# Kernel optimization log

Measured on AMD Instinct MI355X. Metric: run time of the kernel, lower is better.

The kernel has to match this reference:

```python
import jax, jax.numpy as jnp
import numpy as np

DIM = 768
HEADS = 12
HEAD_DIM = DIM // HEADS
HIDDEN = int(DIM * 4.0)
EPS = 1e-5


def _layernorm(x, g, b):
    mu = jnp.mean(x, axis=-1, keepdims=True)
    var = jnp.mean(jnp.square(x - mu), axis=-1, keepdims=True)
    return (x - mu) * jax.lax.rsqrt(var + EPS) * g + b


def setup_inputs() -> dict:
    key = jax.random.key(0)
    ks = jax.random.split(key, 8)
    s_in = 1.0 / np.sqrt(DIM)
    s_hid = 1.0 / np.sqrt(HIDDEN)
    return {
        "x": jax.random.normal(ks[0], (2, 2048, DIM), dtype=jnp.float32),
        "ln1_g": jnp.ones((DIM,), jnp.float32),
        "ln1_b": jnp.zeros((DIM,), jnp.float32),
        "w_qkv": jax.random.normal(ks[1], (DIM, 3 * DIM), jnp.float32) * s_in,
        "w_proj": jax.random.normal(ks[2], (DIM, DIM), jnp.float32) * s_in,
        "b_proj": jnp.zeros((DIM,), jnp.float32),
        "ln2_g": jnp.ones((DIM,), jnp.float32),
        "ln2_b": jnp.zeros((DIM,), jnp.float32),
        "w_fc1": jax.random.normal(ks[3], (DIM, HIDDEN), jnp.float32) * s_in,
        "b_fc1": jnp.zeros((HIDDEN,), jnp.float32),
        "w_fc2": jax.random.normal(ks[4], (HIDDEN, DIM), jnp.float32) * s_hid,
        "b_fc2": jnp.zeros((DIM,), jnp.float32),
    }


def reference(x, ln1_g, ln1_b, w_qkv, w_proj, b_proj, ln2_g, ln2_b, w_fc1, b_fc1, w_fc2, b_fc2):
    b, n, c = x.shape
    scale = HEAD_DIM ** -0.5

    # --- attention branch ---
    h = _layernorm(x, ln1_g, ln1_b)
    qkv = (h @ w_qkv).reshape(b, n, 3, HEADS, HEAD_DIM)
    q, k, v = jnp.moveaxis(qkv, 2, 0)          # each [b, n, H, hd]
    attn = jnp.einsum("bqhd,bkhd->bhqk", q, k) * scale
    attn = jax.nn.softmax(attn, axis=-1)       # [b, H, n, n] (naive, materialized)
    o = jnp.einsum("bhqk,bkhd->bqhd", attn, v).reshape(b, n, c)
    x = x + o @ w_proj + b_proj

    # --- MLP branch ---
    h2 = _layernorm(x, ln2_g, ln2_b)
    m = jax.nn.gelu(h2 @ w_fc1 + b_fc1, approximate=False)
    x = x + m @ w_fc2 + b_fc2
    return x
```

## Files before the change

kernel.cpp:

```cpp
#include <hip/hip_runtime.h>
#include <math.h>


typedef unsigned short u16;
typedef __attribute__((ext_vector_type(8))) short short8;
typedef __attribute__((ext_vector_type(4))) float f32x4;

#define TOKENS 4096
#define DIM    768
#define QKV_N  2304
#define HID    3072
#define NSEQ   2048
#define NHEAD  12
#define HDIM   64

__device__ __forceinline__ float bf2f(u16 u) {
  union { unsigned i; float f; } v; v.i = ((unsigned)u) << 16; return v.f;
}
__device__ __forceinline__ u16 f2bf(float f) {
  union { float f; unsigned i; } v; v.f = f;
  unsigned r = v.i + 0x7fffu + ((v.i >> 16) & 1u);
  return (u16)(r >> 16);
}
__device__ __forceinline__ u16 f2bf_trunc(float f) {
  union { float f; unsigned i; } v; v.f = f;
  return (u16)(v.i >> 16);
}

__device__ __forceinline__ void async_copy16(const u16* g, u16* l) {
  __builtin_amdgcn_global_load_lds(
      (const __attribute__((address_space(1))) unsigned int*)(unsigned long long)g,
      (__attribute__((address_space(3))) unsigned int*)(unsigned int)(unsigned long long)l,
      16, 0, 0);
}

__global__ __launch_bounds__(256) void transpose_all(
    const float* __restrict__ in0, u16* __restrict__ out0,
    const float* __restrict__ in1, u16* __restrict__ out1,
    const float* __restrict__ in2, u16* __restrict__ out2,
    const float* __restrict__ in3, u16* __restrict__ out3) {
  __shared__ u16 t[32][33];
  int bid = blockIdx.x, rem;
  const float* in; u16* out; int R, C;
  if (bid < 1728)      { in = in0; out = out0; R = 768;  C = 2304; rem = bid; }
  else if (bid < 2304) { in = in1; out = out1; R = 768;  C = 768;  rem = bid - 1728; }
  else if (bid < 4608) { in = in2; out = out2; R = 768;  C = 3072; rem = bid - 2304; }
  else                 { in = in3; out = out3; R = 3072; C = 768;  rem = bid - 4608; }
  int c0 = (rem % (C / 32)) * 32, r0 = (rem / (C / 32)) * 32;
  int tx = threadIdx.x, ty = threadIdx.y;
#pragma unroll
  for (int i = 0; i < 4; i++)
    t[ty + i * 8][tx] = f2bf(in[(size_t)(r0 + ty + i * 8) * C + c0 + tx]);
  __syncthreads();
#pragma unroll
  for (int i = 0; i < 4; i++)
    out[(size_t)(c0 + ty + i * 8) * R + r0 + tx] = t[tx][ty + i * 8];
}

__global__ __launch_bounds__(256) void transpose_v(const u16* __restrict__ qkv,
                                                   u16* __restrict__ vt) {
  __shared__ u16 t[32][33];
  int c0 = blockIdx.x * 32;
  int r0 = blockIdx.y * 32;
  int tx = threadIdx.x, ty = threadIdx.y;
#pragma unroll
  for (int i = 0; i < 4; i++)
    t[ty + i * 8][tx] = qkv[(size_t)(r0 + ty + i * 8) * QKV_N + 2 * DIM + c0 + tx];
  __syncthreads();
  int b = r0 >> 11, tok = (r0 & 2047) + tx;
#pragma unroll
  for (int i = 0; i < 4; i++)
    vt[((size_t)b * DIM + c0 + ty + i * 8) * NSEQ + tok] = t[tx][ty + i * 8];
}

template <bool INF32>
__global__ __launch_bounds__(256) void ln_kernel(const void* __restrict__ xin,
                                                 const float* __restrict__ g,
                                                 const float* __restrict__ b,
                                                 u16* __restrict__ out) {
  int wave = threadIdx.x >> 6, lane = threadIdx.x & 63;
  int token = blockIdx.x * 4 + wave;
  float v[12];
  if (INF32) {
    const float4* xr = (const float4*)((const float*)xin + (size_t)token * DIM);
#pragma unroll
    for (int w = 0; w < 3; w++) {
      float4 q = xr[lane + w * 64];
      v[w * 4 + 0] = q.x; v[w * 4 + 1] = q.y; v[w * 4 + 2] = q.z; v[w * 4 + 3] = q.w;
    }
  } else {
    const ushort4* xr = (const ushort4*)((const u16*)xin + (size_t)token * DIM);
#pragma unroll
    for (int w = 0; w < 3; w++) {
      ushort4 q = xr[lane + w * 64];
      v[w * 4 + 0] = bf2f(q.x); v[w * 4 + 1] = bf2f(q.y);
      v[w * 4 + 2] = bf2f(q.z); v[w * 4 + 3] = bf2f(q.w);
    }
  }
  float s = 0.f;
#pragma unroll
  for (int i = 0; i < 12; i++) s += v[i];
#pragma unroll
  for (int off = 32; off > 0; off >>= 1) s += __shfl_xor(s, off);
  float mu = s * (1.0f / DIM);
  float ss = 0.f;
#pragma unroll
  for (int i = 0; i < 12; i++) { float d = v[i] - mu; ss += d * d; }
#pragma unroll
  for (int off = 32; off > 0; off >>= 1) ss += __shfl_xor(ss, off);
  float rs = rsqrtf(ss * (1.0f / DIM) + 1e-5f);

  ushort4* orow = (ushort4*)(out + (size_t)token * DIM);
  const float4* g4 = (const float4*)g;
  const float4* b4 = (const float4*)b;
#pragma unroll
  for (int w = 0; w < 3; w++) {
    float4 gq = g4[lane + w * 64], bq = b4[lane + w * 64];
    ushort4 o;
    o.x = f2bf((v[w * 4 + 0] - mu) * rs * gq.x + bq.x);
    o.y = f2bf((v[w * 4 + 1] - mu) * rs * gq.y + bq.y);
    o.z = f2bf((v[w * 4 + 2] - mu) * rs * gq.z + bq.z);
    o.w = f2bf((v[w * 4 + 3] - mu) * rs * gq.w + bq.w);
    orow[lane + w * 64] = o;
  }
}

template <int BM, int BN, int EPI>
__global__ __launch_bounds__(256, 3) void gemm_bt(
    const u16* __restrict__ A, const u16* __restrict__ BT,
    void* __restrict__ Cout, const float* __restrict__ bias,
    const void* __restrict__ resid, int M, int N, int K) {
  constexpr int MT = BM / 32, NT = BN / 32;
  constexpr int ACH = BM / 16;
  constexpr int CPW = (BM + BN) / 64;
  __shared__ __align__(16) u16 Alds[2][BM * 32];
  __shared__ __align__(16) u16 Blds[2][BN * 32];
  const int tid = threadIdx.x;
  const int lane = tid & 63, wave = tid >> 6;
  const int wr = wave >> 1, wc = wave & 1;
  const int bm = blockIdx.y * BM, bn = blockIdx.x * BN;
  const int c16 = lane & 15, quad = lane >> 4;
  const int l4 = lane >> 2, lc = (lane & 3) * 8;

  f32x4 acc[MT][NT];
#pragma unroll
  for (int i = 0; i < MT; i++)
#pragma unroll
    for (int j = 0; j < NT; j++) acc[i][j] = (f32x4){0.f, 0.f, 0.f, 0.f};

  const u16* gsrc[CPW];
  u16* ldst[CPW];
  int hstep[CPW];
#pragma unroll
  for (int c = 0; c < CPW; c++) {
    int chunk = wave * CPW + c;
    if (chunk < ACH) {
      gsrc[c] = A + (size_t)(bm + chunk * 16 + l4) * K + lc;
      ldst[c] = Alds[0] + chunk * 512;
      hstep[c] = BM * 32;
    } else {
      int bc = chunk - ACH;
      gsrc[c] = BT + (size_t)(bn + bc * 16 + l4) * K + lc;
      ldst[c] = Blds[0] + bc * 512;
      hstep[c] = BN * 32;
    }
  }

  for (int kk = 0; kk < K; kk += 64) {
    __syncthreads();
#pragma unroll
    for (int c = 0; c < CPW; c++) {
      async_copy16(gsrc[c] + kk, ldst[c]);
      async_copy16(gsrc[c] + kk + 32, ldst[c] + hstep[c]);
    }
    __syncthreads();
#pragma unroll
    for (int ks = 0; ks < 2; ks++) {
      short8 af[MT], bfr[NT];
#pragma unroll
      for (int mt = 0; mt < MT; mt++)
        af[mt] = *(const short8*)(Alds[ks] + (wr * (BM / 2) + mt * 16 + c16) * 32 + quad * 8);
#pragma unroll
      for (int nt = 0; nt < NT; nt++)
        bfr[nt] = *(const short8*)(Blds[ks] + (wc * (BN / 2) + nt * 16 + c16) * 32 + quad * 8);
#pragma unroll
      for (int mt = 0; mt < MT; mt++)
#pragma unroll
        for (int nt = 0; nt < NT; nt++)
          acc[mt][nt] = __builtin_amdgcn_mfma_f32_16x16x32_bf16(af[mt], bfr[nt],
                                                                acc[mt][nt], 0, 0, 0);
    }
  }

#pragma unroll
  for (int mt = 0; mt < MT; mt++) {
#pragma unroll
    for (int nt = 0; nt < NT; nt++) {
      int col = bn + wc * (BN / 2) + nt * 16 + c16;
      float bv = (EPI != 0) ? bias[col] : 0.f;
#pragma unroll
      for (int r = 0; r < 4; r++) {
        int row = bm + wr * (BM / 2) + mt * 16 + quad * 4 + r;
        float vv = acc[mt][nt][r];
        if (EPI == 1) {
          vv += bv + ((const float*)resid)[(size_t)row * N + col];
          ((u16*)Cout)[(size_t)row * N + col] = f2bf(vv);
        } else if (EPI == 2) {
          vv += bv;
          vv = 0.5f * vv * (1.0f + erff(vv * 0.70710678118654752f));
          ((u16*)Cout)[(size_t)row * N + col] = f2bf(vv);
        } else if (EPI == 3) {
          vv += bv + bf2f(((const u16*)resid)[(size_t)row * N + col]);
          ((float*)Cout)[(size_t)row * N + col] = vv;
        } else {
          ((u16*)Cout)[(size_t)row * N + col] = f2bf(vv);
        }
      }
    }
  }
}

__global__ __launch_bounds__(128, 2) void attn_kernel(const u16* __restrict__ qkv,
                                                      const u16* __restrict__ vt,
                                                      u16* __restrict__ o) {
  const int tid = threadIdx.x;
  const int lane = tid & 63, wave = tid >> 6;
  const int c16 = lane & 15, quad = lane >> 4;
  const int qt = blockIdx.x & 31;
  const int bh = blockIdx.x >> 5;
  const int bb = bh / NHEAD, h = bh % NHEAD;
  __shared__ __align__(16) u16 Klds[64 * 64];
  __shared__ __align__(16) u16 Vtlds[64 * 64];
  __shared__ __align__(16) u16 Plds[2][2][16 * 64];
  const size_t base = (size_t)bb * NSEQ * QKV_N;
  const int q0 = qt * 64 + wave * 32;

  short8 qf[2][2];
#pragma unroll
  for (int mt = 0; mt < 2; mt++) {
    const u16* qp = qkv + base + (size_t)(q0 + mt * 16 + c16) * QKV_N + h * HDIM;
    qf[mt][0] = *(const short8*)(qp + quad * 8);
    qf[mt][1] = *(const short8*)(qp + 32 + quad * 8);
  }

  float Ls[2][4] = {{0.f, 0.f, 0.f, 0.f}, {0.f, 0.f, 0.f, 0.f}};
  f32x4 Of[2][4];
#pragma unroll
  for (int mt = 0; mt < 2; mt++)
#pragma unroll
    for (int dt = 0; dt < 4; dt++) Of[mt][dt] = (f32x4){0.f, 0.f, 0.f, 0.f};

  const int srow = lane >> 3;
  const int schunk = (lane & 7) ^ srow;
  const int r0 = wave * 32;
  const u16* ksrc = qkv + base + (size_t)(r0 + srow) * QKV_N + DIM + h * HDIM + schunk * 8;
  const u16* vsrc = vt + ((size_t)bh * HDIM + r0 + srow) * NSEQ + schunk * 8;
  u16* kdst = Klds + r0 * 64;
  u16* vdst = Vtlds + r0 * 64;

  const int cswz0 = (quad ^ (c16 & 7)) * 8;
  const int cswz1 = ((quad + 4) ^ (c16 & 7)) * 8;
  const float SC = 0.18033688011112042f;

  for (int kt = 0; kt < NSEQ; kt += 64) {
    __syncthreads();
#pragma unroll
    for (int j = 0; j < 4; j++) {
      async_copy16(ksrc + (size_t)(kt + 8 * j) * QKV_N, kdst + 8 * j * 64);
      async_copy16(vsrc + (size_t)(8 * j) * NSEQ + kt, vdst + 8 * j * 64);
    }
    __syncthreads();

    f32x4 S[2][4];
#pragma unroll
    for (int nt = 0; nt < 4; nt++) {
      const u16* krow = Klds + (nt * 16 + c16) * 64;
      short8 ka = *(const short8*)(krow + cswz0);
      short8 kb = *(const short8*)(krow + cswz1);
#pragma unroll
      for (int mt = 0; mt < 2; mt++) {
        f32x4 s = (f32x4){0.f, 0.f, 0.f, 0.f};
        s = __builtin_amdgcn_mfma_f32_16x16x32_bf16(qf[mt][0], ka, s, 0, 0, 0);
        s = __builtin_amdgcn_mfma_f32_16x16x32_bf16(qf[mt][1], kb, s, 0, 0, 0);
        S[mt][nt] = s;
      }
    }

    const int el = c16 & 7, ch = c16 >> 3;
#pragma unroll
    for (int mt = 0; mt < 2; mt++) {
      u16* pl = Plds[wave][mt];
#pragma unroll
      for (int r = 0; r < 4; r++) {
        float p0 = __builtin_amdgcn_exp2f(S[mt][0][r] * SC);
        float p1 = __builtin_amdgcn_exp2f(S[mt][1][r] * SC);
        float p2 = __builtin_amdgcn_exp2f(S[mt][2][r] * SC);
        float p3 = __builtin_amdgcn_exp2f(S[mt][3][r] * SC);
        Ls[mt][r] += (p0 + p1) + (p2 + p3);
        u16* pr = pl + (quad * 4 + r) * 64;
        const int r7 = (quad * 4 + r) & 7;
        pr[((0 + ch) ^ r7) * 8 + el] = f2bf_trunc(p0);
        pr[((2 + ch) ^ r7) * 8 + el] = f2bf_trunc(p1);
        pr[((4 + ch) ^ r7) * 8 + el] = f2bf_trunc(p2);
        pr[((6 + ch) ^ r7) * 8 + el] = f2bf_trunc(p3);
      }
    }

    short8 pf[2][2];
#pragma unroll
    for (int mt = 0; mt < 2; mt++) {
      const u16* pl = Plds[wave][mt];
      pf[mt][0] = *(const short8*)(pl + c16 * 64 + cswz0);
      pf[mt][1] = *(const short8*)(pl + c16 * 64 + cswz1);
    }
#pragma unroll
    for (int dt = 0; dt < 4; dt++) {
      const u16* vrow = Vtlds + (dt * 16 + c16) * 64;
      short8 va = *(const short8*)(vrow + cswz0);
      short8 vb = *(const short8*)(vrow + cswz1);
#pragma unroll
      for (int mt = 0; mt < 2; mt++) {
        Of[mt][dt] = __builtin_amdgcn_mfma_f32_16x16x32_bf16(pf[mt][0], va, Of[mt][dt], 0, 0, 0);
        Of[mt][dt] = __builtin_amdgcn_mfma_f32_16x16x32_bf16(pf[mt][1], vb, Of[mt][dt], 0, 0, 0);
      }
    }
  }

#pragma unroll
  for (int mt = 0; mt < 2; mt++)
#pragma unroll
    for (int r = 0; r < 4; r++) {
      float t = Ls[mt][r];
      t += __shfl_xor(t, 1); t += __shfl_xor(t, 2);
      t += __shfl_xor(t, 4); t += __shfl_xor(t, 8);
      Ls[mt][r] = t;
    }

#pragma unroll
  for (int mt = 0; mt < 2; mt++)
#pragma unroll
    for (int dt = 0; dt < 4; dt++)
#pragma unroll
      for (int r = 0; r < 4; r++) {
        int token = q0 + mt * 16 + quad * 4 + r;
        float val = Of[mt][dt][r] / Ls[mt][r];
        o[(size_t)(bb * NSEQ + token) * DIM + h * HDIM + dt * 16 + c16] = f2bf(val);
      }
}

extern "C" void kernel_launch(void* const* d_in, const int* in_sizes, int n_in,
                              void* d_out, int out_size, void* d_ws, size_t ws_size,
                              hipStream_t stream) {
  (void)in_sizes; (void)n_in; (void)out_size; (void)ws_size;
  const float* x      = (const float*)d_in[0];
  const float* ln1_g  = (const float*)d_in[1];
  const float* ln1_b  = (const float*)d_in[2];
  const float* w_qkv  = (const float*)d_in[3];
  const float* w_proj = (const float*)d_in[4];
  const float* b_proj = (const float*)d_in[5];
  const float* ln2_g  = (const float*)d_in[6];
  const float* ln2_b  = (const float*)d_in[7];
  const float* w_fc1  = (const float*)d_in[8];
  const float* b_fc1  = (const float*)d_in[9];
  const float* w_fc2  = (const float*)d_in[10];
  const float* b_fc2  = (const float*)d_in[11];
  float* out = (float*)d_out;

  char* p = (char*)d_ws;
  u16* h_bf   = (u16*)p; p += (size_t)TOKENS * DIM * 2;
  u16* qkv_bf = (u16*)p; p += (size_t)TOKENS * QKV_N * 2;
  u16* o_bf   = (u16*)p; p += (size_t)TOKENS * DIM * 2;
  u16* x1_bf  = (u16*)p; p += (size_t)TOKENS * DIM * 2;
  u16* wprojT = (u16*)p; p += (size_t)DIM * DIM * 2;
  u16* wfc1T  = (u16*)p; p += (size_t)HID * DIM * 2;
  u16* wfc2T  = (u16*)p; p += (size_t)DIM * HID * 2;
  u16* wqkvT  = (u16*)p; p += (size_t)QKV_N * DIM * 2;
  u16* vtb    = (u16*)p; p += (size_t)TOKENS * DIM * 2;
  u16* m_bf   = qkv_bf;

  dim3 tb(32, 8);
  transpose_all<<<dim3(6912), tb, 0, stream>>>(w_qkv, wqkvT, w_proj, wprojT,
                                               w_fc1, wfc1T, w_fc2, wfc2T);

  ln_kernel<true><<<TOKENS / 4, 256, 0, stream>>>(x, ln1_g, ln1_b, h_bf);
  gemm_bt<64, 128, 0><<<dim3(QKV_N / 128, TOKENS / 64), 256, 0, stream>>>(
      h_bf, wqkvT, qkv_bf, nullptr, nullptr, TOKENS, QKV_N, DIM);
  transpose_v<<<dim3(DIM / 32, TOKENS / 32), tb, 0, stream>>>(qkv_bf, vtb);
  attn_kernel<<<dim3(2 * NHEAD * (NSEQ / 64)), 128, 0, stream>>>(qkv_bf, vtb, o_bf);
  gemm_bt<64, 128, 1><<<dim3(DIM / 128, TOKENS / 64), 256, 0, stream>>>(
      o_bf, wprojT, x1_bf, b_proj, x, TOKENS, DIM, DIM);
  ln_kernel<false><<<TOKENS / 4, 256, 0, stream>>>(x1_bf, ln2_g, ln2_b, h_bf);
  gemm_bt<128, 128, 2><<<dim3(HID / 128, TOKENS / 128), 256, 0, stream>>>(
      h_bf, wfc1T, m_bf, b_fc1, nullptr, TOKENS, HID, DIM);
  gemm_bt<64, 128, 3><<<dim3(DIM / 128, TOKENS / 64), 256, 0, stream>>>(
      m_bf, wfc2T, out, b_fc2, x1_bf, TOKENS, DIM, HID);
}
```

Measured before the change: 291.6 us.

## Fuse V transpose into QKV GEMM epilogue and double-buffer attention K/V tiles

The QKV GEMM epilogue now writes the V columns directly in transposed layout into the vt buffer, which removes the separate transpose_v kernel and its extra read and write of V. The attention kernel double-buffers the K and Vt LDS tiles and issues async copies for the next tile before computing on the current one, dropping one barrier per iteration so loads overlap with MFMA work. This doubles attention LDS use, which may lower occupancy. The transposed stores are 8-byte strided writes, which may coalesce poorly. Correctness relies on the single barrier at the top of each iteration, together with the async-copy wait behaviour, to order the buffer swaps.

```diff
diff --git a/kernel.cpp b/kernel.cpp
--- a/kernel.cpp
+++ b/kernel.cpp
@@ -57,22 +57,6 @@
     out[(size_t)(c0 + ty + i * 8) * R + r0 + tx] = t[tx][ty + i * 8];
 }
 
-__global__ __launch_bounds__(256) void transpose_v(const u16* __restrict__ qkv,
-                                                   u16* __restrict__ vt) {
-  __shared__ u16 t[32][33];
-  int c0 = blockIdx.x * 32;
-  int r0 = blockIdx.y * 32;
-  int tx = threadIdx.x, ty = threadIdx.y;
-#pragma unroll
-  for (int i = 0; i < 4; i++)
-    t[ty + i * 8][tx] = qkv[(size_t)(r0 + ty + i * 8) * QKV_N + 2 * DIM + c0 + tx];
-  __syncthreads();
-  int b = r0 >> 11, tok = (r0 & 2047) + tx;
-#pragma unroll
-  for (int i = 0; i < 4; i++)
-    vt[((size_t)b * DIM + c0 + ty + i * 8) * NSEQ + tok] = t[tx][ty + i * 8];
-}
-
 template <bool INF32>
 __global__ __launch_bounds__(256) void ln_kernel(const void* __restrict__ xin,
                                                  const float* __restrict__ g,
@@ -129,7 +113,8 @@
 __global__ __launch_bounds__(256, 3) void gemm_bt(
     const u16* __restrict__ A, const u16* __restrict__ BT,
     void* __restrict__ Cout, const float* __restrict__ bias,
-    const void* __restrict__ resid, int M, int N, int K) {
+    const void* __restrict__ resid, int M, int N, int K,
+    u16* __restrict__ vtb) {
   constexpr int MT = BM / 32, NT = BN / 32;
   constexpr int ACH = BM / 16;
   constexpr int CPW = (BM + BN) / 64;
@@ -198,9 +183,18 @@
     for (int nt = 0; nt < NT; nt++) {
       int col = bn + wc * (BN / 2) + nt * 16 + c16;
       float bv = (EPI != 0) ? bias[col] : 0.f;
+      int row0 = bm + wr * (BM / 2) + mt * 16 + quad * 4;
+      if (EPI == 0 && col >= 2 * DIM) {
+        int b = row0 >> 11;
+        ushort4 pk;
+        pk.x = f2bf(acc[mt][nt][0]); pk.y = f2bf(acc[mt][nt][1]);
+        pk.z = f2bf(acc[mt][nt][2]); pk.w = f2bf(acc[mt][nt][3]);
+        *(ushort4*)(vtb + ((size_t)b * DIM + col - 2 * DIM) * NSEQ + (row0 & 2047)) = pk;
+        continue;
+      }
 #pragma unroll
       for (int r = 0; r < 4; r++) {
-        int row = bm + wr * (BM / 2) + mt * 16 + quad * 4 + r;
+        int row = row0 + r;
         float vv = acc[mt][nt][r];
         if (EPI == 1) {
           vv += bv + ((const float*)resid)[(size_t)row * N + col];
@@ -229,8 +223,8 @@
   const int qt = blockIdx.x & 31;
   const int bh = blockIdx.x >> 5;
   const int bb = bh / NHEAD, h = bh % NHEAD;
-  __shared__ __align__(16) u16 Klds[64 * 64];
-  __shared__ __align__(16) u16 Vtlds[64 * 64];
+  __shared__ __align__(16) u16 Klds[2][64 * 64];
+  __shared__ __align__(16) u16 Vtlds[2][64 * 64];
   __shared__ __align__(16) u16 Plds[2][2][16 * 64];
   const size_t base = (size_t)bb * NSEQ * QKV_N;
   const int q0 = qt * 64 + wave * 32;
@@ -255,26 +249,35 @@
   const int r0 = wave * 32;
   const u16* ksrc = qkv + base + (size_t)(r0 + srow) * QKV_N + DIM + h * HDIM + schunk * 8;
   const u16* vsrc = vt + ((size_t)bh * HDIM + r0 + srow) * NSEQ + schunk * 8;
-  u16* kdst = Klds + r0 * 64;
-  u16* vdst = Vtlds + r0 * 64;
 
   const int cswz0 = (quad ^ (c16 & 7)) * 8;
   const int cswz1 = ((quad + 4) ^ (c16 & 7)) * 8;
   const float SC = 0.18033688011112042f;
 
-  for (int kt = 0; kt < NSEQ; kt += 64) {
+#pragma unroll
+  for (int j = 0; j < 4; j++) {
+    async_copy16(ksrc + (size_t)(8 * j) * QKV_N, Klds[0] + r0 * 64 + 8 * j * 64);
+    async_copy16(vsrc + (size_t)(8 * j) * NSEQ, Vtlds[0] + r0 * 64 + 8 * j * 64);
+  }
+
+  for (int it = 0; it < NSEQ / 64; it++) {
+    const int cur = it & 1;
     __syncthreads();
-#pragma unroll
-    for (int j = 0; j < 4; j++) {
-      async_copy16(ksrc + (size_t)(kt + 8 * j) * QKV_N, kdst + 8 * j * 64);
-      async_copy16(vsrc + (size_t)(8 * j) * NSEQ + kt, vdst + 8 * j * 64);
-    }
-    __syncthreads();
+    if (it + 1 < NSEQ / 64) {
+      const int kt1 = (it + 1) * 64;
+      u16* kd = Klds[cur ^ 1] + r0 * 64;
+      u16* vd = Vtlds[cur ^ 1] + r0 * 64;
+#pragma unroll
+      for (int j = 0; j < 4; j++) {
+        async_copy16(ksrc + (size_t)(kt1 + 8 * j) * QKV_N, kd + 8 * j * 64);
+        async_copy16(vsrc + (size_t)(8 * j) * NSEQ + kt1, vd + 8 * j * 64);
+      }
+    }
 
     f32x4 S[2][4];
 #pragma unroll
     for (int nt = 0; nt < 4; nt++) {
-      const u16* krow = Klds + (nt * 16 + c16) * 64;
+      const u16* krow = Klds[cur] + (nt * 16 + c16) * 64;
       short8 ka = *(const short8*)(krow + cswz0);
       short8 kb = *(const short8*)(krow + cswz1);
 #pragma unroll
@@ -315,7 +318,7 @@
     }
 #pragma unroll
     for (int dt = 0; dt < 4; dt++) {
-      const u16* vrow = Vtlds + (dt * 16 + c16) * 64;
+      const u16* vrow = Vtlds[cur] + (dt * 16 + c16) * 64;
       short8 va = *(const short8*)(vrow + cswz0);
       short8 vb = *(const short8*)(vrow + cswz1);
 #pragma unroll
@@ -384,14 +387,13 @@
 
   ln_kernel<true><<<TOKENS / 4, 256, 0, stream>>>(x, ln1_g, ln1_b, h_bf);
   gemm_bt<64, 128, 0><<<dim3(QKV_N / 128, TOKENS / 64), 256, 0, stream>>>(
-      h_bf, wqkvT, qkv_bf, nullptr, nullptr, TOKENS, QKV_N, DIM);
-  transpose_v<<<dim3(DIM / 32, TOKENS / 32), tb, 0, stream>>>(qkv_bf, vtb);
+      h_bf, wqkvT, qkv_bf, nullptr, nullptr, TOKENS, QKV_N, DIM, vtb);
   attn_kernel<<<dim3(2 * NHEAD * (NSEQ / 64)), 128, 0, stream>>>(qkv_bf, vtb, o_bf);
   gemm_bt<64, 128, 1><<<dim3(DIM / 128, TOKENS / 64), 256, 0, stream>>>(
-      o_bf, wprojT, x1_bf, b_proj, x, TOKENS, DIM, DIM);
+      o_bf, wprojT, x1_bf, b_proj, x, TOKENS, DIM, DIM, nullptr);
   ln_kernel<false><<<TOKENS / 4, 256, 0, stream>>>(x1_bf, ln2_g, ln2_b, h_bf);
   gemm_bt<128, 128, 2><<<dim3(HID / 128, TOKENS / 128), 256, 0, stream>>>(
-      h_bf, wfc1T, m_bf, b_fc1, nullptr, TOKENS, HID, DIM);
+      h_bf, wfc1T, m_bf, b_fc1, nullptr, TOKENS, HID, DIM, nullptr);
   gemm_bt<64, 128, 3><<<dim3(DIM / 128, TOKENS / 64), 256, 0, stream>>>(
-      m_bf, wfc2T, out, b_fc2, x1_bf, TOKENS, DIM, HID);
-}
+      m_bf, wfc2T, out, b_fc2, x1_bf, TOKENS, DIM, HID, nullptr);
+}
```

Result: faster. 276.7 us (-5.1%).
